# Optimization experiments

Hardware: AMD Instinct MI355X
Metric: run time of the kernel (lower is better)

Reference implementation:

```python
import jax, jax.numpy as jnp
import numpy as np

B, N, D, H = 4, 2048, 1024, 16
Dh = D // H
ROPE_THETA = 10000.0


def _rope(x):
    # x: [b, h, n, d]; interleaved rotary (lucidrains rotary_embedding_torch style)
    n, d = x.shape[-2], x.shape[-1]
    inv_freq = 1.0 / (ROPE_THETA ** (jnp.arange(0, d, 2, dtype=jnp.float32) / d))
    freqs = jnp.arange(n, dtype=jnp.float32)[:, None] * inv_freq[None, :]  # [n, d/2]
    freqs = jnp.repeat(freqs, 2, axis=-1)  # [n, d], interleaved
    cos, sin = jnp.cos(freqs), jnp.sin(freqs)
    x1 = x[..., ::2]
    x2 = x[..., 1::2]
    rot = jnp.stack([-x2, x1], axis=-1).reshape(x.shape)  # rotate_half, interleaved
    return x * cos + rot * sin


def setup_inputs() -> dict:
    key = jax.random.key(0)
    ks = jax.random.split(key, 9)
    s = 0.02
    return {
        "x": jax.random.normal(ks[0], (B, N, D), dtype=jnp.float32),
        "Wq": jax.random.normal(ks[1], (D, D), dtype=jnp.float32) * s,
        "bq": jax.random.normal(ks[2], (D,), dtype=jnp.float32) * s,
        "Wk": jax.random.normal(ks[3], (D, D), dtype=jnp.float32) * s,
        "bk": jax.random.normal(ks[4], (D,), dtype=jnp.float32) * s,
        "Wv": jax.random.normal(ks[5], (D, D), dtype=jnp.float32) * s,
        "bv": jax.random.normal(ks[6], (D,), dtype=jnp.float32) * s,
        "Wo": jax.random.normal(ks[7], (D, D), dtype=jnp.float32) * s,
        "bo": jax.random.normal(ks[8], (D,), dtype=jnp.float32) * s,
    }


def reference(x, Wq, bq, Wk, bk, Wv, bv, Wo, bo):
    b, n, d = x.shape
    split = lambda t: t.reshape(b, n, H, Dh).transpose(0, 2, 1, 3)  # b h n d
    q = split(x @ Wq + bq)
    k = split(x @ Wk + bk)
    v = split(x @ Wv + bv)
    q = _rope(q)
    k = _rope(k)
    # NOTE: source scales by 1/sqrt(Dh * num_heads) == 1/sqrt(dim)
    scores = jnp.einsum('bhnd,bhmd->bhnm', q, k) / jnp.sqrt(jnp.float32(d))
    weights = jax.nn.softmax(scores, axis=-1)
    inter = jnp.einsum('bhnm,bhmd->bhnd', weights, v)
    inter = inter.transpose(0, 2, 1, 3).reshape(b, n, d)  # b n (h d)
    return inter @ Wo + bo
```

## Files before the change

### kernel.cpp

```cpp
#include <hip/hip_runtime.h>

#define DEV __device__ __forceinline__

#define VMCNT(N) asm volatile("s_waitcnt vmcnt(" #N ")" ::: "memory")
#define SBAR()                              \
  do {                                      \
    __builtin_amdgcn_sched_barrier(0);      \
    __builtin_amdgcn_s_barrier();           \
    __builtin_amdgcn_sched_barrier(0);      \
  } while (0)

typedef __attribute__((ext_vector_type(4))) float f32x4;
typedef __attribute__((ext_vector_type(16))) float f32x16;
typedef __attribute__((ext_vector_type(4))) float fl4;
typedef __attribute__((ext_vector_type(8))) __bf16 bf16x8;
typedef __attribute__((ext_vector_type(2))) __bf16 bf16x2;
typedef __attribute__((ext_vector_type(4))) unsigned short us4;
typedef __attribute__((ext_vector_type(8))) unsigned short us8;
typedef __attribute__((ext_vector_type(4))) unsigned int ui4;

DEV unsigned short f2bf(float f) {
  unsigned u = __builtin_bit_cast(unsigned, f);
  u += 0x7fffu + ((u >> 16) & 1u);
  return (unsigned short)(u >> 16);
}
DEV float bf2f(unsigned short h) {
  unsigned u = ((unsigned)h) << 16;
  return __builtin_bit_cast(float, u);
}

DEV void load_lds16(const void* g, void* l) {
  __builtin_amdgcn_global_load_lds(
      (const __attribute__((address_space(1))) void*)g,
      (__attribute__((address_space(3))) void*)l, 16, 0, 0);
}

DEV unsigned pk2(float a, float b) {
  bf16x2 t;
  t[0] = (__bf16)a; t[1] = (__bf16)b;
  return __builtin_bit_cast(unsigned, t);
}
DEV bf16x8 frag4(unsigned a, unsigned b, unsigned c, unsigned d) {
  ui4 u; u[0] = a; u[1] = b; u[2] = c; u[3] = d;
  return __builtin_bit_cast(bf16x8, u);
}

__global__ void k_convert_x(const float* __restrict__ x, unsigned short* __restrict__ xb) {
  size_t i = (size_t)blockIdx.x * 256 + threadIdx.x;
  const float* p = x + i * 8;
  fl4 a = *(const fl4*)p;
  fl4 b = *(const fl4*)(p + 4);
  us8 o;
  o[0] = f2bf(a[0]); o[1] = f2bf(a[1]); o[2] = f2bf(a[2]); o[3] = f2bf(a[3]);
  o[4] = f2bf(b[0]); o[5] = f2bf(b[1]); o[6] = f2bf(b[2]); o[7] = f2bf(b[3]);
  *(us8*)(xb + i * 8) = o;
}

__global__ void k_tab(float2* __restrict__ tab) {
  int i = blockIdx.x * 256 + threadIdx.x;
  int pos = i >> 5, t = i & 31;
  float ang = (float)pos * exp2f(-(float)t * 0.41524101186092029f);
  float sn, cs;
  __sincosf(ang, &sn, &cs);
  tab[i] = make_float2(cs, sn);
}

__global__ void k_transw(const float* __restrict__ W0, const float* __restrict__ W1,
                         const float* __restrict__ W2, const float* __restrict__ W3,
                         unsigned short* __restrict__ T0, unsigned short* __restrict__ T1,
                         unsigned short* __restrict__ T2, unsigned short* __restrict__ T3) {
  const float* W; unsigned short* T;
  switch (blockIdx.y) {
    case 0: W = W0; T = T0; break;
    case 1: W = W1; T = T1; break;
    case 2: W = W2; T = T2; break;
    default: W = W3; T = T3; break;
  }
  __shared__ float tile[64][65];
  int k0 = (blockIdx.x >> 4) * 64, n0 = (blockIdx.x & 15) * 64;
  int tr = threadIdx.x >> 4, tc = (threadIdx.x & 15) * 4;
#pragma unroll
  for (int p = 0; p < 4; ++p) {
    int r = p * 16 + tr;
    fl4 v = *(const fl4*)&W[(size_t)(k0 + r) * 1024 + n0 + tc];
#pragma unroll
    for (int j = 0; j < 4; ++j) tile[r][tc + j] = v[j];
  }
  __syncthreads();
#pragma unroll
  for (int p = 0; p < 4; ++p) {
    int rr = p * 16 + tr;
    us4 o;
#pragma unroll
    for (int j = 0; j < 4; ++j) o[j] = f2bf(tile[tc + j][rr]);
    *(us4*)&T[(size_t)(n0 + rr) * 1024 + k0 + tc] = o;
  }
}

__global__ __launch_bounds__(256, 3) void k_gemm_qkv(
    const unsigned short* __restrict__ A, const unsigned short* __restrict__ Bt,
    const float* __restrict__ bq, const float* __restrict__ bk, const float* __restrict__ bv,
    const float2* __restrict__ tab,
    unsigned short* __restrict__ Qb, unsigned short* __restrict__ Kb,
    unsigned short* __restrict__ Vt) {
  __shared__ alignas(16) unsigned short As[3][4096];
  __shared__ alignas(16) unsigned short Bs[3][4096];
  const int tid = threadIdx.x, w = tid >> 6, l = tid & 63;
  const int lg = l >> 4, lm = l & 15;
  const int sw = (blockIdx.x & 7) * 192 + (blockIdx.x >> 3);
  const int bm = sw / 24, bn = sw - bm * 24;
  const int wr = w >> 1, wc = w & 1;
  f32x4 acc[4][4] = {};

  auto stage = [&](int buf, int kt) {
#pragma unroll
    for (int p = 0; p < 2; ++p) {
      int cb = (w * 2 + p) * 64, c = cb + l, g = c >> 7, r = c & 127;
      load_lds16(A + (size_t)(bm * 128 + r) * 1024 + kt * 32 + g * 8, &As[buf][cb * 8]);
      load_lds16(Bt + (size_t)(bn * 128 + r) * 1024 + kt * 32 + g * 8, &Bs[buf][cb * 8]);
    }
  };
  stage(0, 0);
  stage(1, 1);
  int cur = 0;
  for (int kt = 0; kt < 32; ++kt) {
    if (kt == 31) VMCNT(0); else VMCNT(4);
    SBAR();
    if (kt + 2 < 32) {
      int nb = cur + 2; if (nb >= 3) nb -= 3;
      stage(nb, kt + 2);
    }
    bf16x8 af[4], bfr[4];
#pragma unroll
    for (int m = 0; m < 4; ++m)
      af[m] = *(const bf16x8*)&As[cur][(lg * 128 + wr * 64 + m * 16 + lm) * 8];
#pragma unroll
    for (int n = 0; n < 4; ++n)
      bfr[n] = *(const bf16x8*)&Bs[cur][(lg * 128 + wc * 64 + n * 16 + lm) * 8];
    __builtin_amdgcn_s_setprio(1);
#pragma unroll
    for (int m = 0; m < 4; ++m)
#pragma unroll
      for (int n = 0; n < 4; ++n)
        acc[m][n] = __builtin_amdgcn_mfma_f32_16x16x32_bf16(af[m], bfr[n], acc[m][n], 0, 0, 0);
    __builtin_amdgcn_s_setprio(0);
    cur = (cur == 2) ? 0 : cur + 1;
  }
  const int row0 = bm * 128 + wr * 64;
  const int col0 = bn * 128 + wc * 64;
  const int seg = bn >> 3;
  if (seg == 2) {
#pragma unroll
    for (int n = 0; n < 4; ++n) {
      int hd = (col0 & 1023) + n * 16 + lm;
      float bvv = bv[hd];
#pragma unroll
      for (int m = 0; m < 4; ++m) {
        int row = row0 + m * 16 + lg * 4;
        int bb = row >> 11, s = row & 2047;
        us4 o;
#pragma unroll
        for (int i = 0; i < 4; ++i) o[i] = f2bf(acc[m][n][i] + bvv);
        *(us4*)&Vt[((size_t)(bb * 1024 + hd)) * 2048 + s] = o;
      }
    }
  } else {
    const float* bias = seg ? bk : bq;
    unsigned short* Dst = seg ? Kb : Qb;
    const float qsc = seg ? 1.0f : 0.045084220027780106f;
#pragma unroll
    for (int n = 0; n < 4; ++n) {
      int ch = (col0 & 1023) + n * 16 + lm;
      int t = (ch & 63) >> 1;
      float bvv = bias[ch];
#pragma unroll
      for (int m = 0; m < 4; ++m) {
#pragma unroll
        for (int i = 0; i < 4; ++i) {
          int row = row0 + m * 16 + lg * 4 + i;
          int pos = row & 2047;
          float xv = bf2f(f2bf(acc[m][n][i] + bvv));
          float xp = __shfl_xor(xv, 1, 64);
          float2 cs = tab[pos * 32 + t];
          float out = (lm & 1) ? (xv * cs.x + xp * cs.y) * qsc
                               : (xv * cs.x - xp * cs.y) * qsc;
          Dst[(size_t)row * 1024 + ch] = f2bf(out);
        }
      }
    }
  }
}

__global__ __launch_bounds__(256, 3) void k_gemm_o(const unsigned short* __restrict__ A,
                                                   const unsigned short* __restrict__ Bt,
                                                   const float* __restrict__ bias,
                                                   float* __restrict__ C) {
  __shared__ alignas(16) unsigned short As[3][4096];
  __shared__ alignas(16) unsigned short Bs[3][4096];
  const int tid = threadIdx.x, w = tid >> 6, l = tid & 63;
  const int lg = l >> 4, lm = l & 15;
  const int sw = (blockIdx.x & 7) * 64 + (blockIdx.x >> 3);
  const int bm = sw >> 3, bn = sw & 7;
  const int wr = w >> 1, wc = w & 1;
  f32x4 acc[4][4] = {};
  auto stage = [&](int buf, int kt) {
#pragma unroll
    for (int p = 0; p < 2; ++p) {
      int cb = (w * 2 + p) * 64, c = cb + l, g = c >> 7, r = c & 127;
      load_lds16(A + (size_t)(bm * 128 + r) * 1024 + kt * 32 + g * 8, &As[buf][cb * 8]);
      load_lds16(Bt + (size_t)(bn * 128 + r) * 1024 + kt * 32 + g * 8, &Bs[buf][cb * 8]);
    }
  };
  stage(0, 0);
  stage(1, 1);
  int cur = 0;
  for (int kt = 0; kt < 32; ++kt) {
    if (kt == 31) VMCNT(0); else VMCNT(4);
    SBAR();
    if (kt + 2 < 32) {
      int nb = cur + 2; if (nb >= 3) nb -= 3;
      stage(nb, kt + 2);
    }
    bf16x8 af[4], bfr[4];
#pragma unroll
    for (int m = 0; m < 4; ++m)
      af[m] = *(const bf16x8*)&As[cur][(lg * 128 + wr * 64 + m * 16 + lm) * 8];
#pragma unroll
    for (int n = 0; n < 4; ++n)
      bfr[n] = *(const bf16x8*)&Bs[cur][(lg * 128 + wc * 64 + n * 16 + lm) * 8];
    __builtin_amdgcn_s_setprio(1);
#pragma unroll
    for (int m = 0; m < 4; ++m)
#pragma unroll
      for (int n = 0; n < 4; ++n)
        acc[m][n] = __builtin_amdgcn_mfma_f32_16x16x32_bf16(af[m], bfr[n], acc[m][n], 0, 0, 0);
    __builtin_amdgcn_s_setprio(0);
    cur = (cur == 2) ? 0 : cur + 1;
  }
  const int row0 = bm * 128 + wr * 64, col0 = bn * 128 + wc * 64;
#pragma unroll
  for (int n = 0; n < 4; ++n) {
    int col = col0 + n * 16 + lm;
    float bv = bias[col];
#pragma unroll
    for (int m = 0; m < 4; ++m) {
      int row = row0 + m * 16 + lg * 4;
#pragma unroll
      for (int i = 0; i < 4; ++i)
        C[(size_t)(row + i) * 1024 + col] = acc[m][n][i] + bv;
    }
  }
}

__global__ __launch_bounds__(512, 4) void k_attn(const unsigned short* __restrict__ Q,
                                                 const unsigned short* __restrict__ K,
                                                 const unsigned short* __restrict__ Vt,
                                                 unsigned short* __restrict__ O) {
  __shared__ alignas(16) unsigned short Ks[3][4096];
  __shared__ alignas(16) unsigned short Vs[3][4096];
  const int tid = threadIdx.x, w = tid >> 6, l = tid & 63;
  const int lq = l & 31, hi = l >> 5;
  const int bid = (blockIdx.x & 7) * 64 + (blockIdx.x >> 3);
  const int qt = bid & 7, h = (bid >> 3) & 15, b = bid >> 7;
  const int qrow = qt * 256 + w * 32 + lq;

  const unsigned short* qp = Q + ((size_t)(b * 2048 + qrow)) * 1024 + h * 64 + hi * 8;
  bf16x8 qf[4];
#pragma unroll
  for (int dc = 0; dc < 4; ++dc) qf[dc] = *(const bf16x8*)(qp + dc * 16);

  const unsigned short* Kbase = K + ((size_t)(b * 2048)) * 1024 + h * 64;
  const unsigned short* Vbase = Vt + ((size_t)((b * 16 + h) * 64)) * 2048;
  const int sg = tid >> 6, sl = tid & 63;
  const size_t koff = ((size_t)((sg >> 2) * 32 + (sl & 31))) * 1024 + (sg & 3) * 16 + (sl >> 5) * 8;
  const size_t voff = ((size_t)((sg & 1) * 32 + (sl & 31))) * 2048 + (sg >> 1) * 16 + (sl >> 5) * 8;

  auto stageKV = [&](int buf, int tt) {
    load_lds16(Kbase + (size_t)(tt * 64) * 1024 + koff, &Ks[buf][tid * 8]);
    load_lds16(Vbase + tt * 64 + voff, &Vs[buf][tid * 8]);
  };

  float M = -1e30f, L = 0.0f;
  f32x16 Oa0 = {}, Oa1 = {};

  stageKV(0, 0);
  stageKV(1, 1);
  int cur = 0;
  for (int t = 0; t < 32; ++t) {
    if (t == 31) VMCNT(0); else VMCNT(2);
    SBAR();
    if (t + 2 < 32) {
      int nb = cur + 2; if (nb >= 3) nb -= 3;
      stageKV(nb, t + 2);
    }
    f32x16 s0 = {}, s1 = {};
    const unsigned short* Kc = Ks[cur];
    __builtin_amdgcn_s_setprio(1);
#pragma unroll
    for (int dc = 0; dc < 4; ++dc) {
      bf16x8 kf0 = *(const bf16x8*)&Kc[(dc * 64 + l) * 8];
      bf16x8 kf1 = *(const bf16x8*)&Kc[((4 + dc) * 64 + l) * 8];
      s0 = __builtin_amdgcn_mfma_f32_32x32x16_bf16(kf0, qf[dc], s0, 0, 0, 0);
      s1 = __builtin_amdgcn_mfma_f32_32x32x16_bf16(kf1, qf[dc], s1, 0, 0, 0);
    }
    __builtin_amdgcn_s_setprio(0);
    float mx = s0[0];
#pragma unroll
    for (int r = 1; r < 15; r += 2) mx = fmaxf(fmaxf(mx, s0[r]), s0[r + 1]);
    mx = fmaxf(mx, s0[15]);
#pragma unroll
    for (int r = 0; r < 16; r += 2) mx = fmaxf(fmaxf(mx, s1[r]), s1[r + 1]);
    mx = fmaxf(mx, __shfl_xor(mx, 32, 64));
    if (!__all(mx - M <= 8.0f)) {
      const float nm = fmaxf(M, mx);
      const float sc = exp2f(M - nm);
      L *= sc;
      Oa0 *= sc;
      Oa1 *= sc;
      M = nm;
    }
#pragma unroll
    for (int r = 0; r < 16; ++r) s0[r] = exp2f(s0[r] - M);
#pragma unroll
    for (int r = 0; r < 16; ++r) s1[r] = exp2f(s1[r] - M);
    float q8[8];
#pragma unroll
    for (int j = 0; j < 8; ++j) q8[j] = (s0[j] + s0[j + 8]) + (s1[j] + s1[j + 8]);
#pragma unroll
    for (int j = 0; j < 4; ++j) q8[j] += q8[j + 4];
    float ls = (q8[0] + q8[1]) + (q8[2] + q8[3]);
    ls += __shfl_xor(ls, 32, 64);
    L += ls;
    unsigned w0[8], w1[8];
#pragma unroll
    for (int j = 0; j < 8; ++j) {
      w0[j] = pk2(s0[2 * j], s0[2 * j + 1]);
      w1[j] = pk2(s1[2 * j], s1[2 * j + 1]);
    }
    unsigned ra = __shfl_xor(hi ? w0[0] : w0[2], 32, 64);
    unsigned rb = __shfl_xor(hi ? w0[1] : w0[3], 32, 64);
    unsigned rc = __shfl_xor(hi ? w0[4] : w0[6], 32, 64);
    unsigned rd = __shfl_xor(hi ? w0[5] : w0[7], 32, 64);
    unsigned re = __shfl_xor(hi ? w1[0] : w1[2], 32, 64);
    unsigned rf = __shfl_xor(hi ? w1[1] : w1[3], 32, 64);
    unsigned rg = __shfl_xor(hi ? w1[4] : w1[6], 32, 64);
    unsigned rh = __shfl_xor(hi ? w1[5] : w1[7], 32, 64);
    bf16x8 pf0 = hi ? frag4(ra, rb, w0[2], w0[3]) : frag4(w0[0], w0[1], ra, rb);
    bf16x8 pf1 = hi ? frag4(rc, rd, w0[6], w0[7]) : frag4(w0[4], w0[5], rc, rd);
    bf16x8 pf2 = hi ? frag4(re, rf, w1[2], w1[3]) : frag4(w1[0], w1[1], re, rf);
    bf16x8 pf3 = hi ? frag4(rg, rh, w1[6], w1[7]) : frag4(w1[4], w1[5], rg, rh);
    const unsigned short* Vc = Vs[cur];
    __builtin_amdgcn_s_setprio(1);
    {
      bf16x8 v0 = *(const bf16x8*)&Vc[(0 * 64 + l) * 8];
      bf16x8 v1 = *(const bf16x8*)&Vc[(1 * 64 + l) * 8];
      Oa0 = __builtin_amdgcn_mfma_f32_32x32x16_bf16(v0, pf0, Oa0, 0, 0, 0);
      Oa1 = __builtin_amdgcn_mfma_f32_32x32x16_bf16(v1, pf0, Oa1, 0, 0, 0);
      v0 = *(const bf16x8*)&Vc[(2 * 64 + l) * 8];
      v1 = *(const bf16x8*)&Vc[(3 * 64 + l) * 8];
      Oa0 = __builtin_amdgcn_mfma_f32_32x32x16_bf16(v0, pf1, Oa0, 0, 0, 0);
      Oa1 = __builtin_amdgcn_mfma_f32_32x32x16_bf16(v1, pf1, Oa1, 0, 0, 0);
      v0 = *(const bf16x8*)&Vc[(4 * 64 + l) * 8];
      v1 = *(const bf16x8*)&Vc[(5 * 64 + l) * 8];
      Oa0 = __builtin_amdgcn_mfma_f32_32x32x16_bf16(v0, pf2, Oa0, 0, 0, 0);
      Oa1 = __builtin_amdgcn_mfma_f32_32x32x16_bf16(v1, pf2, Oa1, 0, 0, 0);
      v0 = *(const bf16x8*)&Vc[(6 * 64 + l) * 8];
      v1 = *(const bf16x8*)&Vc[(7 * 64 + l) * 8];
      Oa0 = __builtin_amdgcn_mfma_f32_32x32x16_bf16(v0, pf3, Oa0, 0, 0, 0);
      Oa1 = __builtin_amdgcn_mfma_f32_32x32x16_bf16(v1, pf3, Oa1, 0, 0, 0);
    }
    __builtin_amdgcn_s_setprio(0);
    cur = (cur == 2) ? 0 : cur + 1;
  }
  const float inv = 1.0f / L;
  unsigned short* op = O + ((size_t)(b * 2048 + qrow)) * 1024 + h * 64;
#pragma unroll
  for (int gq = 0; gq < 4; ++gq) {
    const int d0 = 8 * gq + 4 * hi;
    us4 o0, o1;
#pragma unroll
    for (int i = 0; i < 4; ++i) {
      o0[i] = f2bf(Oa0[gq * 4 + i] * inv);
      o1[i] = f2bf(Oa1[gq * 4 + i] * inv);
    }
    *(us4*)&op[d0] = o0;
    *(us4*)&op[32 + d0] = o1;
  }
}

extern "C" void kernel_launch(void* const* d_in, const int* in_sizes, int n_in,
                              void* d_out, int out_size, void* d_ws, size_t ws_size,
                              hipStream_t stream) {
  const float* x  = (const float*)d_in[0];
  const float* Wq = (const float*)d_in[1];
  const float* bq = (const float*)d_in[2];
  const float* Wk = (const float*)d_in[3];
  const float* bk = (const float*)d_in[4];
  const float* Wv = (const float*)d_in[5];
  const float* bv = (const float*)d_in[6];
  const float* Wo = (const float*)d_in[7];
  const float* bo = (const float*)d_in[8];

  unsigned short* xb   = (unsigned short*)d_ws;
  unsigned short* Wqkv = xb + (size_t)8192 * 1024;
  unsigned short* WoT  = Wqkv + (size_t)3072 * 1024;
  unsigned short* Qb   = WoT + (size_t)1024 * 1024;
  unsigned short* Kb   = Qb + (size_t)8192 * 1024;
  unsigned short* Vt   = Kb + (size_t)8192 * 1024;
  unsigned short* Ib   = Vt + (size_t)8192 * 1024;
  float2* tab = (float2*)Ib;

  k_convert_x<<<4096, 256, 0, stream>>>(x, xb);
  k_tab<<<256, 256, 0, stream>>>(tab);
  k_transw<<<dim3(256, 4), 256, 0, stream>>>(
      Wq, Wk, Wv, Wo, Wqkv, Wqkv + (size_t)1024 * 1024, Wqkv + (size_t)2048 * 1024, WoT);
  k_gemm_qkv<<<1536, 256, 0, stream>>>(xb, Wqkv, bq, bk, bv, tab, Qb, Kb, Vt);
  k_attn<<<512, 512, 0, stream>>>(Qb, Kb, Vt, Ib);
  k_gemm_o<<<512, 256, 0, stream>>>(Ib, WoT, bo, (float*)d_out);
}
```

Measured before the change: 276.4 us.

## Merge prep kernels into one launch and shrink attention blocks to 256 threads

Three preprocessing kernels (x conversion, RoPE table, weight transposes) become a single launch that dispatches on block index, which removes two kernel launches. The attention kernel now uses 4 waves per block covering 128 query rows with 1024 blocks instead of 8 waves over 256 rows. The K/V pipeline goes from triple-buffered with vmcnt waits to double buffering with __syncthreads, and each thread issues two loads per tensor. This gives more blocks and less LDS per block, but each block re-reads K/V for fewer queries, so K/V traffic roughly doubles, and the simpler sync may expose more load latency.

```diff
diff --git a/kernel.cpp b/kernel.cpp
--- a/kernel.cpp
+++ b/kernel.cpp
@@ -45,55 +45,58 @@
   return __builtin_bit_cast(bf16x8, u);
 }
 
-__global__ void k_convert_x(const float* __restrict__ x, unsigned short* __restrict__ xb) {
-  size_t i = (size_t)blockIdx.x * 256 + threadIdx.x;
-  const float* p = x + i * 8;
-  fl4 a = *(const fl4*)p;
-  fl4 b = *(const fl4*)(p + 4);
-  us8 o;
-  o[0] = f2bf(a[0]); o[1] = f2bf(a[1]); o[2] = f2bf(a[2]); o[3] = f2bf(a[3]);
-  o[4] = f2bf(b[0]); o[5] = f2bf(b[1]); o[6] = f2bf(b[2]); o[7] = f2bf(b[3]);
-  *(us8*)(xb + i * 8) = o;
-}
-
-__global__ void k_tab(float2* __restrict__ tab) {
-  int i = blockIdx.x * 256 + threadIdx.x;
-  int pos = i >> 5, t = i & 31;
-  float ang = (float)pos * exp2f(-(float)t * 0.41524101186092029f);
-  float sn, cs;
-  __sincosf(ang, &sn, &cs);
-  tab[i] = make_float2(cs, sn);
-}
-
-__global__ void k_transw(const float* __restrict__ W0, const float* __restrict__ W1,
-                         const float* __restrict__ W2, const float* __restrict__ W3,
-                         unsigned short* __restrict__ T0, unsigned short* __restrict__ T1,
-                         unsigned short* __restrict__ T2, unsigned short* __restrict__ T3) {
-  const float* W; unsigned short* T;
-  switch (blockIdx.y) {
-    case 0: W = W0; T = T0; break;
-    case 1: W = W1; T = T1; break;
-    case 2: W = W2; T = T2; break;
-    default: W = W3; T = T3; break;
-  }
+__global__ void k_prep(const float* __restrict__ x, unsigned short* __restrict__ xb,
+                       float2* __restrict__ tab,
+                       const float* __restrict__ W0, const float* __restrict__ W1,
+                       const float* __restrict__ W2, const float* __restrict__ W3,
+                       unsigned short* __restrict__ T0, unsigned short* __restrict__ T1,
+                       unsigned short* __restrict__ T2, unsigned short* __restrict__ T3) {
   __shared__ float tile[64][65];
-  int k0 = (blockIdx.x >> 4) * 64, n0 = (blockIdx.x & 15) * 64;
-  int tr = threadIdx.x >> 4, tc = (threadIdx.x & 15) * 4;
-#pragma unroll
-  for (int p = 0; p < 4; ++p) {
-    int r = p * 16 + tr;
-    fl4 v = *(const fl4*)&W[(size_t)(k0 + r) * 1024 + n0 + tc];
-#pragma unroll
-    for (int j = 0; j < 4; ++j) tile[r][tc + j] = v[j];
-  }
-  __syncthreads();
-#pragma unroll
-  for (int p = 0; p < 4; ++p) {
-    int rr = p * 16 + tr;
-    us4 o;
-#pragma unroll
-    for (int j = 0; j < 4; ++j) o[j] = f2bf(tile[tc + j][rr]);
-    *(us4*)&T[(size_t)(n0 + rr) * 1024 + k0 + tc] = o;
+  const int bx = blockIdx.x, tid = threadIdx.x;
+  if (bx < 4096) {
+    size_t i = (size_t)bx * 256 + tid;
+    const float* p = x + i * 8;
+    fl4 a = *(const fl4*)p;
+    fl4 b = *(const fl4*)(p + 4);
+    us8 o;
+    o[0] = f2bf(a[0]); o[1] = f2bf(a[1]); o[2] = f2bf(a[2]); o[3] = f2bf(a[3]);
+    o[4] = f2bf(b[0]); o[5] = f2bf(b[1]); o[6] = f2bf(b[2]); o[7] = f2bf(b[3]);
+    *(us8*)(xb + i * 8) = o;
+  } else if (bx < 4352) {
+    int i = (bx - 4096) * 256 + tid;
+    int pos = i >> 5, t = i & 31;
+    float ang = (float)pos * exp2f(-(float)t * 0.41524101186092029f);
+    float sn, cs;
+    __sincosf(ang, &sn, &cs);
+    tab[i] = make_float2(cs, sn);
+  } else {
+    int bid = bx - 4352;
+    const float* W; unsigned short* T;
+    switch (bid >> 8) {
+      case 0: W = W0; T = T0; break;
+      case 1: W = W1; T = T1; break;
+      case 2: W = W2; T = T2; break;
+      default: W = W3; T = T3; break;
+    }
+    int bxy = bid & 255;
+    int k0 = (bxy >> 4) * 64, n0 = (bxy & 15) * 64;
+    int tr = tid >> 4, tc = (tid & 15) * 4;
+#pragma unroll
+    for (int p = 0; p < 4; ++p) {
+      int r = p * 16 + tr;
+      fl4 v = *(const fl4*)&W[(size_t)(k0 + r) * 1024 + n0 + tc];
+#pragma unroll
+      for (int j = 0; j < 4; ++j) tile[r][tc + j] = v[j];
+    }
+    __syncthreads();
+#pragma unroll
+    for (int p = 0; p < 4; ++p) {
+      int rr = p * 16 + tr;
+      us4 o;
+#pragma unroll
+      for (int j = 0; j < 4; ++j) o[j] = f2bf(tile[tc + j][rr]);
+      *(us4*)&T[(size_t)(n0 + rr) * 1024 + k0 + tc] = o;
+    }
   }
 }
 
@@ -252,17 +255,17 @@
   }
 }
 
-__global__ __launch_bounds__(512, 4) void k_attn(const unsigned short* __restrict__ Q,
+__global__ __launch_bounds__(256, 4) void k_attn(const unsigned short* __restrict__ Q,
                                                  const unsigned short* __restrict__ K,
                                                  const unsigned short* __restrict__ Vt,
                                                  unsigned short* __restrict__ O) {
-  __shared__ alignas(16) unsigned short Ks[3][4096];
-  __shared__ alignas(16) unsigned short Vs[3][4096];
+  __shared__ alignas(16) unsigned short Ks[2][4096];
+  __shared__ alignas(16) unsigned short Vs[2][4096];
   const int tid = threadIdx.x, w = tid >> 6, l = tid & 63;
   const int lq = l & 31, hi = l >> 5;
-  const int bid = (blockIdx.x & 7) * 64 + (blockIdx.x >> 3);
-  const int qt = bid & 7, h = (bid >> 3) & 15, b = bid >> 7;
-  const int qrow = qt * 256 + w * 32 + lq;
+  const int bid = (blockIdx.x & 7) * 128 + (blockIdx.x >> 3);
+  const int qt = bid & 15, h = (bid >> 4) & 15, b = bid >> 8;
+  const int qrow = qt * 128 + w * 32 + lq;
 
   const unsigned short* qp = Q + ((size_t)(b * 2048 + qrow)) * 1024 + h * 64 + hi * 8;
   bf16x8 qf[4];
@@ -271,28 +274,27 @@
 
   const unsigned short* Kbase = K + ((size_t)(b * 2048)) * 1024 + h * 64;
   const unsigned short* Vbase = Vt + ((size_t)((b * 16 + h) * 64)) * 2048;
-  const int sg = tid >> 6, sl = tid & 63;
-  const size_t koff = ((size_t)((sg >> 2) * 32 + (sl & 31))) * 1024 + (sg & 3) * 16 + (sl >> 5) * 8;
-  const size_t voff = ((size_t)((sg & 1) * 32 + (sl & 31))) * 2048 + (sg >> 1) * 16 + (sl >> 5) * 8;
+  const int g0 = tid >> 6, ll = tid & 63;
+  const size_t koff = ((size_t)((g0 >> 2) * 32 + (ll & 31))) * 1024 + (g0 & 3) * 16 + (ll >> 5) * 8;
+  const size_t voff = ((size_t)((g0 & 1) * 32 + (ll & 31))) * 2048 + (g0 >> 1) * 16 + (ll >> 5) * 8;
 
   auto stageKV = [&](int buf, int tt) {
-    load_lds16(Kbase + (size_t)(tt * 64) * 1024 + koff, &Ks[buf][tid * 8]);
+    const size_t kb = (size_t)(tt * 64) * 1024;
+    load_lds16(Kbase + kb + koff, &Ks[buf][tid * 8]);
+    load_lds16(Kbase + kb + koff + (size_t)32 * 1024, &Ks[buf][(tid + 256) * 8]);
     load_lds16(Vbase + tt * 64 + voff, &Vs[buf][tid * 8]);
+    load_lds16(Vbase + tt * 64 + voff + 32, &Vs[buf][(tid + 256) * 8]);
   };
 
   float M = -1e30f, L = 0.0f;
   f32x16 Oa0 = {}, Oa1 = {};
 
   stageKV(0, 0);
-  stageKV(1, 1);
-  int cur = 0;
+  __syncthreads();
+
   for (int t = 0; t < 32; ++t) {
-    if (t == 31) VMCNT(0); else VMCNT(2);
-    SBAR();
-    if (t + 2 < 32) {
-      int nb = cur + 2; if (nb >= 3) nb -= 3;
-      stageKV(nb, t + 2);
-    }
+    const int cur = t & 1;
+    if (t < 31) stageKV(cur ^ 1, t + 1);
     f32x16 s0 = {}, s1 = {};
     const unsigned short* Kc = Ks[cur];
     __builtin_amdgcn_s_setprio(1);
@@ -370,7 +372,7 @@
       Oa1 = __builtin_amdgcn_mfma_f32_32x32x16_bf16(v1, pf3, Oa1, 0, 0, 0);
     }
     __builtin_amdgcn_s_setprio(0);
-    cur = (cur == 2) ? 0 : cur + 1;
+    if (t < 31) __syncthreads();
   }
   const float inv = 1.0f / L;
   unsigned short* op = O + ((size_t)(b * 2048 + qrow)) * 1024 + h * 64;
@@ -410,11 +412,10 @@
   unsigned short* Ib   = Vt + (size_t)8192 * 1024;
   float2* tab = (float2*)Ib;
 
-  k_convert_x<<<4096, 256, 0, stream>>>(x, xb);
-  k_tab<<<256, 256, 0, stream>>>(tab);
-  k_transw<<<dim3(256, 4), 256, 0, stream>>>(
-      Wq, Wk, Wv, Wo, Wqkv, Wqkv + (size_t)1024 * 1024, Wqkv + (size_t)2048 * 1024, WoT);
+  k_prep<<<5376, 256, 0, stream>>>(x, xb, tab, Wq, Wk, Wv, Wo,
+                                   Wqkv, Wqkv + (size_t)1024 * 1024,
+                                   Wqkv + (size_t)2048 * 1024, WoT);
   k_gemm_qkv<<<1536, 256, 0, stream>>>(xb, Wqkv, bq, bk, bv, tab, Qb, Kb, Vt);
-  k_attn<<<512, 512, 0, stream>>>(Qb, Kb, Vt, Ib);
+  k_attn<<<1024, 256, 0, stream>>>(Qb, Kb, Vt, Ib);
   k_gemm_o<<<512, 256, 0, stream>>>(Ib, WoT, bo, (float*)d_out);
 }
```

New measurement: 273.8 us. Within noise of the previous version (-0.9%).
